# Kernel optimization log

Measured on AMD Instinct MI355X. Metric: run time of the kernel, lower is better.

The kernel has to match this reference:

```python
import jax, jax.numpy as jnp
import numpy as np

B, S, E, H = 4, 2048, 1024, 16
D = E // H  # head_dim = 64


def setup_inputs() -> dict:
    key = jax.random.key(0)
    ks = jax.random.split(key, 5)
    return {
        "x": jax.random.normal(ks[0], (B, S, E), dtype=jnp.float32),
        "w_qkv": jax.random.normal(ks[1], (3 * E, E), dtype=jnp.float32) * (E ** -0.5),
        "b_qkv": jax.random.normal(ks[2], (3 * E,), dtype=jnp.float32) * 0.02,
        "w_proj": jax.random.normal(ks[3], (E, E), dtype=jnp.float32) * (E ** -0.5),
        "b_proj": jax.random.normal(ks[4], (E,), dtype=jnp.float32) * 0.02,
    }


def reference(x, w_qkv, b_qkv, w_proj, b_proj):
    # fused QKV projection: [B,S,E] -> [B,S,3E] -> [B,S,3,H,D]
    qkv = (jnp.einsum("bse,fe->bsf", x, w_qkv) + b_qkv).reshape(B, S, 3, H, D)
    q, k, v = qkv[:, :, 0], qkv[:, :, 1], qkv[:, :, 2]  # each [B,S,H,D]
    scale = 1.0 / jnp.sqrt(jnp.asarray(D, dtype=q.dtype))
    scores = jnp.einsum("bqhd,bkhd->bhqk", q, k) * scale  # [B,H,S,S]
    attn = jax.nn.softmax(scores, axis=-1)
    out = jnp.einsum("bhqk,bkhd->bqhd", attn, v).reshape(B, S, E)
    return jnp.einsum("bse,fe->bsf", out, w_proj) + b_proj
```

## Files before the change

kernel.cpp:

```cpp
#include <hip/hip_runtime.h>
#include <cstdint>
#include <cstddef>

#define B_ 4
#define S_ 2048
#define E_ 1024
#define H_ 16
#define D_ 64
#define M_ (B_*S_)
#define NE_ ((size_t)B_*H_*S_*D_)

typedef unsigned int  u32;
typedef unsigned short u16;
typedef __attribute__((ext_vector_type(8))) short bf16x8;
typedef __attribute__((ext_vector_type(4))) float f32x4;
typedef __attribute__((ext_vector_type(2))) unsigned int u32x2;

__device__ __forceinline__ u16 f2bf(float x) {
    u32 u = __float_as_uint(x);
    u32 r = (u + 0x7FFFu + ((u >> 16) & 1u)) >> 16;
    return (u16)r;
}
__device__ __forceinline__ float bf2f(u16 h) { return __uint_as_float((u32)h << 16); }

__device__ __forceinline__ u32 cvtpk_bf16(float lo, float hi) {
    u32 r;
    asm("v_cvt_pk_bf16_f32 %0, %1, %2" : "=v"(r) : "v"(lo), "v"(hi));
    return r;
}

__device__ __forceinline__ void gload_lds16(const void* gsrc, void* lds) {
    __builtin_amdgcn_global_load_lds(
        (const __attribute__((address_space(1))) u32*)gsrc,
        (__attribute__((address_space(3))) u32*)lds, 16, 0, 0);
}


__global__ __launch_bounds__(256)
void convert_img(const float* __restrict__ src, u16* __restrict__ dh, u16* __restrict__ dl)
{
    const int tile = blockIdx.x;
    const int rt = tile >> 5, kt = tile & 31;
    const size_t tb = (size_t)tile * 2048;
    const int ci = threadIdx.x;
    const int l  = ci >> 3;
    const int ph = ci & 7;
    const int s  = ph ^ (l & 7);
    const int r  = (l << 1) | (s >> 2);
    const int k0 = (s & 3) << 3;
    const float* sp = src + ((size_t)(rt * 64 + r)) * 1024 + kt * 32 + k0;
    const float4 f0 = *(const float4*)sp;
    const float4 f1 = *(const float4*)(sp + 4);
    const float vals[8] = {f0.x, f0.y, f0.z, f0.w, f1.x, f1.y, f1.z, f1.w};
    __align__(16) short hs[8];
    __align__(16) short ls[8];
    #pragma unroll
    for (int j = 0; j < 8; ++j) {
        const u16 h = f2bf(vals[j]);
        hs[j] = (short)h;
        ls[j] = (short)f2bf(vals[j] - bf2f(h));
    }
    *(bf16x8*)(dh + tb + ci * 8) = *(const bf16x8*)hs;
    *(bf16x8*)(dl + tb + ci * 8) = *(const bf16x8*)ls;
}

template<int MODE>
__global__ __launch_bounds__(512, 1)
void gemm_mfma(const u16* __restrict__ AIh, const u16* __restrict__ AIl,
               const u16* __restrict__ BIh, const u16* __restrict__ BIl,
               const float* __restrict__ bias, float* __restrict__ Cout,
               u16* __restrict__ qh, u16* __restrict__ ql,
               u16* __restrict__ kh,
               u16* __restrict__ vh, u16* __restrict__ vl)
{
    __shared__ __align__(16) u16 sT[3][12][2048];

    constexpr int GY = (MODE == 0) ? 24 : 8;
    constexpr int NCH = (32 * GY) >> 3;

    const int tid = threadIdx.x, lane = tid & 63, w = tid >> 6;
    const int quad = lane >> 4, l15 = lane & 15;

    const int flat = blockIdx.x;
    const int swz  = (flat & 7) * NCH + (flat >> 3);
    const int bx   = swz / GY, by = swz % GY;

    const int m0  = bx * 256;
    const int n0  = by * 128;
    const int mt0 = bx * 4;
    const int nt0 = by * 2;
    const int rw  = w >> 1;
    const int cw  = w & 1;

    const u16* srcq[6];
    #pragma unroll
    for (int it = 0; it < 6; ++it) {
        const int g = w * 6 + it;
        const int t = g >> 2, qtr = g & 3;
        const u16* img = (t < 4) ? AIh : (t < 8) ? AIl : (t < 10) ? BIh : BIl;
        const int rtile = (t < 8) ? (mt0 + (t & 3)) : (nt0 + (t & 1));
        srcq[it] = img + (size_t)rtile * (32 * 2048) + qtr * 512 + lane * 8;
    }

    f32x4 acc[4][4];
    #pragma unroll
    for (int i = 0; i < 4; ++i)
        #pragma unroll
        for (int j = 0; j < 4; ++j)
            acc[i][j] = (f32x4){0.f, 0.f, 0.f, 0.f};

    #pragma unroll
    for (int it = 0; it < 6; ++it)
        gload_lds16(srcq[it], (char*)&sT[0][0][0] + (w * 6 + it) * 1024);
    #pragma unroll
    for (int it = 0; it < 6; ++it)
        gload_lds16(srcq[it] + 2048, (char*)&sT[1][0][0] + (w * 6 + it) * 1024);

    int cb = 0;
    for (int kt = 0; kt < 32; ++kt) {
        if (kt < 31) asm volatile("s_waitcnt vmcnt(6)" ::: "memory");
        else         asm volatile("s_waitcnt vmcnt(0)" ::: "memory");
        asm volatile("s_barrier" ::: "memory");

        if (kt + 2 < 32) {
            int nb = cb + 2; if (nb >= 3) nb -= 3;
            #pragma unroll
            for (int it = 0; it < 6; ++it)
                gload_lds16(srcq[it] + (size_t)(kt + 2) * 2048,
                            (char*)&sT[nb][0][0] + (w * 6 + it) * 1024);
        }

        bf16x8 aH[4], aL[4], bH[4], bL[4];
        #pragma unroll
        for (int i = 0; i < 4; ++i) {
            const int r = i * 16 + l15, l = r >> 1;
            const int off = l * 64 + (((((r & 1) << 2) + quad) ^ (l & 7)) << 3);
            aH[i] = *(const bf16x8*)&sT[cb][rw][off];
            aL[i] = *(const bf16x8*)&sT[cb][4 + rw][off];
        }
        #pragma unroll
        for (int j = 0; j < 4; ++j) {
            const int r = j * 16 + l15, l = r >> 1;
            const int off = l * 64 + (((((r & 1) << 2) + quad) ^ (l & 7)) << 3);
            bH[j] = *(const bf16x8*)&sT[cb][8 + cw][off];
            bL[j] = *(const bf16x8*)&sT[cb][10 + cw][off];
        }

        __builtin_amdgcn_s_setprio(1);
        #pragma unroll
        for (int i = 0; i < 4; ++i)
            #pragma unroll
            for (int j = 0; j < 4; ++j) {
                acc[i][j] = __builtin_amdgcn_mfma_f32_16x16x32_bf16(aL[i], bH[j], acc[i][j], 0, 0, 0);
                acc[i][j] = __builtin_amdgcn_mfma_f32_16x16x32_bf16(aH[i], bL[j], acc[i][j], 0, 0, 0);
                acc[i][j] = __builtin_amdgcn_mfma_f32_16x16x32_bf16(aH[i], bH[j], acc[i][j], 0, 0, 0);
            }
        __builtin_amdgcn_s_setprio(0);

        cb += 1; if (cb >= 3) cb = 0;
    }

    const int fbase = n0 + cw * 64;
    float bj[4];
    #pragma unroll
    for (int j = 0; j < 4; ++j) bj[j] = bias[fbase + j * 16 + l15];

    if (MODE == 0) {
        const int cR = fbase >> 10;
        const int hh = (fbase >> 6) & 15;
        #pragma unroll
        for (int i = 0; i < 4; ++i)
            #pragma unroll
            for (int j = 0; j < 4; ++j)
                #pragma unroll
                for (int reg = 0; reg < 4; ++reg) {
                    float val = acc[i][j][reg] + bj[j];
                    const int m = m0 + rw * 64 + i * 16 + quad * 4 + reg;
                    const int d = j * 16 + l15;
                    const int bb = m >> 11, s = m & 2047;
                    const int bh = bb * 16 + hh;
                    if (cR == 0) val *= 0.18033688011112042f;
                    const u16 h = f2bf(val);
                    if (cR == 0) {
                        const u16 lo = f2bf(val - bf2f(h));
                        const size_t idx = ((size_t)bh * 2048 + s) * 64 + d;
                        qh[idx] = h; ql[idx] = lo;
                    } else if (cR == 1) {
                        const size_t tile = (size_t)bh * 32 + (s >> 6);
                        const int r = s & 63;
                        const size_t off = (tile << 12) + r * 64 + (((d >> 3) ^ (r & 7)) << 3) + (d & 7);
                        kh[off] = h;
                    } else {
                        const u16 lo = f2bf(val - bf2f(h));
                        const size_t tile = (size_t)bh * 32 + (s >> 6);
                        const size_t off = (tile << 12) + d * 64 + ((((s & 63) >> 3) ^ (d & 7)) << 3) + (s & 7);
                        vh[off] = h; vl[off] = lo;
                    }
                }
    } else {
        #pragma unroll
        for (int i = 0; i < 4; ++i)
            #pragma unroll
            for (int j = 0; j < 4; ++j)
                #pragma unroll
                for (int reg = 0; reg < 4; ++reg) {
                    const int m = m0 + rw * 64 + i * 16 + quad * 4 + reg;
                    const int f = fbase + j * 16 + l15;
                    Cout[(size_t)m * 1024 + f] = acc[i][j][reg] + bj[j];
                }
    }
}

__global__ __launch_bounds__(256, 3)
void attn_mfma(const u16* __restrict__ qh, const u16* __restrict__ ql,
               const u16* __restrict__ kh,
               const u16* __restrict__ vh, const u16* __restrict__ vl,
               u16* __restrict__ oh, u16* __restrict__ ol)
{
    __shared__ __align__(16) u16 KV[3][4096];

    const int tid  = threadIdx.x;
    const int lane = tid & 63, w = tid >> 6;
    const int quad = lane >> 4, l15 = lane & 15;
    const int bh = blockIdx.y;
    const int q0 = blockIdx.x * 128 + w * 32;

    bf16x8 Qf[2][2][2];
    #pragma unroll
    for (int qs = 0; qs < 2; ++qs)
        #pragma unroll
        for (int kk = 0; kk < 2; ++kk) {
            const size_t idx = ((size_t)bh * S_ + q0 + qs * 16 + l15) * 64 + kk * 32 + quad * 8;
            Qf[qs][kk][0] = *(const bf16x8*)(qh + idx);
            Qf[qs][kk][1] = *(const bf16x8*)(ql + idx);
        }

    f32x4 O[2][4];
    float l_part[2] = {0.f, 0.f};
    #pragma unroll
    for (int qs = 0; qs < 2; ++qs)
        #pragma unroll
        for (int ds = 0; ds < 4; ++ds)
            O[qs][ds] = (f32x4){0.f, 0.f, 0.f, 0.f};

    const char* gk[3] = {(const char*)kh, (const char*)vh, (const char*)vl};

    for (int kt = 0; kt < S_ / 64; ++kt) {
        __syncthreads();
        const size_t tb = (((size_t)bh * 32 + kt) << 13);
        #pragma unroll
        for (int a = 0; a < 3; ++a)
            #pragma unroll
            for (int it = 0; it < 2; ++it) {
                const int off = w * 2048 + it * 1024;
                gload_lds16(gk[a] + tb + off + lane * 16, (char*)&KV[a][0] + off);
            }
        __syncthreads();

        f32x4 S[2][4];
        #pragma unroll
        for (int qs = 0; qs < 2; ++qs)
            #pragma unroll
            for (int ks = 0; ks < 4; ++ks)
                S[qs][ks] = (f32x4){-23.083120654223414f, -23.083120654223414f,
                                    -23.083120654223414f, -23.083120654223414f};

        __builtin_amdgcn_s_setprio(1);
        #pragma unroll
        for (int ks = 0; ks < 4; ++ks) {
            const int r = ks * 16 + l15;
            #pragma unroll
            for (int kk = 0; kk < 2; ++kk) {
                const int c = (kk * 4 + quad) ^ (r & 7);
                const bf16x8 Kh = *(const bf16x8*)&KV[0][r * 64 + c * 8];
                #pragma unroll
                for (int qs = 0; qs < 2; ++qs) {
                    S[qs][ks] = __builtin_amdgcn_mfma_f32_16x16x32_bf16(Kh, Qf[qs][kk][1], S[qs][ks], 0, 0, 0);
                    S[qs][ks] = __builtin_amdgcn_mfma_f32_16x16x32_bf16(Kh, Qf[qs][kk][0], S[qs][ks], 0, 0, 0);
                }
            }
        }
        __builtin_amdgcn_s_setprio(0);

        u32 PA[2][2][4];
        #pragma unroll
        for (int qs = 0; qs < 2; ++qs) {
            float lsum = 0.f;
            u32 PK[4][2];
            #pragma unroll
            for (int ks = 0; ks < 4; ++ks) {
                const float p0 = __builtin_exp2f(S[qs][ks][0]);
                const float p1 = __builtin_exp2f(S[qs][ks][1]);
                const float p2 = __builtin_exp2f(S[qs][ks][2]);
                const float p3 = __builtin_exp2f(S[qs][ks][3]);
                lsum += (p0 + p1) + (p2 + p3);
                PK[ks][0] = cvtpk_bf16(p0, p1);
                PK[ks][1] = cvtpk_bf16(p2, p3);
            }
            l_part[qs] += lsum;
            #pragma unroll
            for (int kk = 0; kk < 2; ++kk) {
                const u32x2 t0 = __builtin_amdgcn_permlane32_swap(PK[2 * kk][0], PK[2 * kk + 1][0], false, false);
                const u32x2 w02 = __builtin_amdgcn_permlane16_swap(t0.x, t0.y, false, false);
                const u32x2 t1 = __builtin_amdgcn_permlane32_swap(PK[2 * kk][1], PK[2 * kk + 1][1], false, false);
                const u32x2 w13 = __builtin_amdgcn_permlane16_swap(t1.x, t1.y, false, false);
                PA[qs][kk][0] = w02.x;
                PA[qs][kk][1] = w13.x;
                PA[qs][kk][2] = w02.y;
                PA[qs][kk][3] = w13.y;
            }
        }

        __builtin_amdgcn_s_setprio(1);
        #pragma unroll
        for (int kk = 0; kk < 2; ++kk) {
            union { u32 w4[4]; bf16x8 v; } pu0, pu1;
            #pragma unroll
            for (int c = 0; c < 4; ++c) { pu0.w4[c] = PA[0][kk][c]; pu1.w4[c] = PA[1][kk][c]; }
            const bf16x8 paf[2] = {pu0.v, pu1.v};
            #pragma unroll
            for (int ds = 0; ds < 4; ++ds) {
                const int r = ds * 16 + l15;
                const int c = (kk * 4 + quad) ^ (r & 7);
                const bf16x8 Vh = *(const bf16x8*)&KV[1][r * 64 + c * 8];
                const bf16x8 Vl = *(const bf16x8*)&KV[2][r * 64 + c * 8];
                #pragma unroll
                for (int qs = 0; qs < 2; ++qs) {
                    O[qs][ds] = __builtin_amdgcn_mfma_f32_16x16x32_bf16(Vl, paf[qs], O[qs][ds], 0, 0, 0);
                    O[qs][ds] = __builtin_amdgcn_mfma_f32_16x16x32_bf16(Vh, paf[qs], O[qs][ds], 0, 0, 0);
                }
            }
        }
        __builtin_amdgcn_s_setprio(0);
    }

    float linv[2];
    #pragma unroll
    for (int qs = 0; qs < 2; ++qs) {
        float rs = l_part[qs];
        rs += __shfl_xor(rs, 16);
        rs += __shfl_xor(rs, 32);
        linv[qs] = 1.f / rs;
    }

    const int bb = bh >> 4, hh = bh & 15;
    #pragma unroll
    for (int qs = 0; qs < 2; ++qs) {
        const float inv = linv[qs];
        const int s = q0 + qs * 16 + l15;
        const int m = bb * 2048 + s;
        const int mt = m >> 6, r = m & 63;
        const int l = r >> 1;
        const size_t tb0 = ((size_t)(mt * 32 + hh * 2)) * 2048;
        #pragma unroll
        for (int ds = 0; ds < 4; ++ds) {
            const int d0 = ds * 16 + quad * 4;
            const float v0 = O[qs][ds][0] * inv;
            const float v1 = O[qs][ds][1] * inv;
            const float v2 = O[qs][ds][2] * inv;
            const float v3 = O[qs][ds][3] * inv;
            const u32 h01 = cvtpk_bf16(v0, v1);
            const u32 h23 = cvtpk_bf16(v2, v3);
            const float r0 = v0 - bf2f((u16)h01);
            const float r1 = v1 - bf2f((u16)(h01 >> 16));
            const float r2 = v2 - bf2f((u16)h23);
            const float r3 = v3 - bf2f((u16)(h23 >> 16));
            const u32 l01 = cvtpk_bf16(r0, r1);
            const u32 l23 = cvtpk_bf16(r2, r3);
            const int c  = (d0 & 31) >> 3;
            const int ph = (((r & 1) << 2) + c) ^ (l & 7);
            const size_t off = tb0 + (size_t)(d0 >> 5) * 2048 + l * 64 + ph * 8 + (d0 & 7);
            *(u32x2*)(oh + off) = (u32x2){h01, h23};
            *(u32x2*)(ol + off) = (u32x2){l01, l23};
        }
    }
}

extern "C" void kernel_launch(void* const* d_in, const int* in_sizes, int n_in,
                              void* d_out, int out_size, void* d_ws, size_t ws_size,
                              hipStream_t stream) {
    const float* x      = (const float*)d_in[0];
    const float* w_qkv  = (const float*)d_in[1];
    const float* b_qkv  = (const float*)d_in[2];
    const float* w_proj = (const float*)d_in[3];
    const float* b_proj = (const float*)d_in[4];
    float* out = (float*)d_out;

    u16* qh  = (u16*)d_ws;
    u16* ql  = qh + NE_;
    u16* kh  = ql + NE_;
    u16* vh  = kh + NE_;
    u16* vl  = vh + NE_;
    u16* xh  = vl + NE_;
    u16* xl  = xh + NE_;
    u16* wqh = xl + NE_;
    u16* wql = wqh + (size_t)3 * 1024 * 1024;
    u16* oh  = xh;
    u16* ol  = xl;
    u16* wph = wqh;
    u16* wpl = wph + (size_t)1024 * 1024;

    convert_img<<<128 * 32, 256, 0, stream>>>(x, xh, xl);
    convert_img<<<48 * 32, 256, 0, stream>>>(w_qkv, wqh, wql);

    {
        dim3 grid(32 * 24);
        gemm_mfma<0><<<grid, 512, 0, stream>>>(xh, xl, wqh, wql,
                                               b_qkv, nullptr, qh, ql, kh, vh, vl);
    }
    {
        dim3 grid(S_ / 128, B_ * H_);
        attn_mfma<<<grid, 256, 0, stream>>>(qh, ql, kh, vh, vl, oh, ol);
    }
    convert_img<<<16 * 32, 256, 0, stream>>>(w_proj, wph, wpl);
    {
        dim3 grid(32 * 8);
        gemm_mfma<1><<<grid, 512, 0, stream>>>(oh, ol, wph, wpl,
                                               b_proj, out, nullptr, nullptr, nullptr,
                                               nullptr, nullptr);
    }
}
```

Before: 444.3 us.

## Split output projection into dedicated double-buffered GEMM kernel with two blocks per CU

The templated GEMM is split into a QKV kernel and a separate projection kernel. The projection kernel uses a two-stage LDS buffer instead of three, which frees enough shared memory for launch bounds of two 512-thread blocks per CU. It also drops the swizzled 1D grid in favour of a plain 2D grid and syncs every k-step. The aim is more occupancy on the small 256-block projection GEMM, at the cost of less prefetch depth and an extra barrier per iteration.

```diff
diff --git a/kernel.cpp b/kernel.cpp
--- a/kernel.cpp
+++ b/kernel.cpp
@@ -64,18 +64,17 @@
     *(bf16x8*)(dl + tb + ci * 8) = *(const bf16x8*)ls;
 }
 
-template<int MODE>
 __global__ __launch_bounds__(512, 1)
-void gemm_mfma(const u16* __restrict__ AIh, const u16* __restrict__ AIl,
-               const u16* __restrict__ BIh, const u16* __restrict__ BIl,
-               const float* __restrict__ bias, float* __restrict__ Cout,
-               u16* __restrict__ qh, u16* __restrict__ ql,
-               u16* __restrict__ kh,
-               u16* __restrict__ vh, u16* __restrict__ vl)
+void gemm_qkv(const u16* __restrict__ AIh, const u16* __restrict__ AIl,
+              const u16* __restrict__ BIh, const u16* __restrict__ BIl,
+              const float* __restrict__ bias,
+              u16* __restrict__ qh, u16* __restrict__ ql,
+              u16* __restrict__ kh,
+              u16* __restrict__ vh, u16* __restrict__ vl)
 {
     __shared__ __align__(16) u16 sT[3][12][2048];
 
-    constexpr int GY = (MODE == 0) ? 24 : 8;
+    constexpr int GY = 24;
     constexpr int NCH = (32 * GY) >> 3;
 
     const int tid = threadIdx.x, lane = tid & 63, w = tid >> 6;
@@ -165,50 +164,129 @@
     #pragma unroll
     for (int j = 0; j < 4; ++j) bj[j] = bias[fbase + j * 16 + l15];
 
-    if (MODE == 0) {
-        const int cR = fbase >> 10;
-        const int hh = (fbase >> 6) & 15;
+    const int cR = fbase >> 10;
+    const int hh = (fbase >> 6) & 15;
+    #pragma unroll
+    for (int i = 0; i < 4; ++i)
+        #pragma unroll
+        for (int j = 0; j < 4; ++j)
+            #pragma unroll
+            for (int reg = 0; reg < 4; ++reg) {
+                float val = acc[i][j][reg] + bj[j];
+                const int m = m0 + rw * 64 + i * 16 + quad * 4 + reg;
+                const int d = j * 16 + l15;
+                const int bb = m >> 11, s = m & 2047;
+                const int bh = bb * 16 + hh;
+                if (cR == 0) val *= 0.18033688011112042f;
+                const u16 h = f2bf(val);
+                if (cR == 0) {
+                    const u16 lo = f2bf(val - bf2f(h));
+                    const size_t idx = ((size_t)bh * 2048 + s) * 64 + d;
+                    qh[idx] = h; ql[idx] = lo;
+                } else if (cR == 1) {
+                    const size_t tile = (size_t)bh * 32 + (s >> 6);
+                    const int r = s & 63;
+                    const size_t off = (tile << 12) + r * 64 + (((d >> 3) ^ (r & 7)) << 3) + (d & 7);
+                    kh[off] = h;
+                } else {
+                    const u16 lo = f2bf(val - bf2f(h));
+                    const size_t tile = (size_t)bh * 32 + (s >> 6);
+                    const size_t off = (tile << 12) + d * 64 + ((((s & 63) >> 3) ^ (d & 7)) << 3) + (s & 7);
+                    vh[off] = h; vl[off] = lo;
+                }
+            }
+}
+
+__global__ __launch_bounds__(512, 2)
+void gemm_proj(const u16* __restrict__ AIh, const u16* __restrict__ AIl,
+               const u16* __restrict__ BIh, const u16* __restrict__ BIl,
+               const float* __restrict__ bias, float* __restrict__ Cout)
+{
+    __shared__ __align__(16) u16 sT[2][12][2048];
+
+    const int tid = threadIdx.x, lane = tid & 63, w = tid >> 6;
+    const int quad = lane >> 4, l15 = lane & 15;
+    const int bx = blockIdx.x, by = blockIdx.y;
+    const int m0  = bx * 256;
+    const int n0  = by * 128;
+    const int mt0 = bx * 4;
+    const int nt0 = by * 2;
+    const int rw  = w >> 1;
+    const int cw  = w & 1;
+
+    const u16* srcq[6];
+    #pragma unroll
+    for (int it = 0; it < 6; ++it) {
+        const int g = w * 6 + it;
+        const int t = g >> 2, qtr = g & 3;
+        const u16* img = (t < 4) ? AIh : (t < 8) ? AIl : (t < 10) ? BIh : BIl;
+        const int rtile = (t < 8) ? (mt0 + (t & 3)) : (nt0 + (t & 1));
+        srcq[it] = img + (size_t)rtile * (32 * 2048) + qtr * 512 + lane * 8;
+    }
+
+    f32x4 acc[4][4];
+    #pragma unroll
+    for (int i = 0; i < 4; ++i)
+        #pragma unroll
+        for (int j = 0; j < 4; ++j)
+            acc[i][j] = (f32x4){0.f, 0.f, 0.f, 0.f};
+
+    #pragma unroll
+    for (int it = 0; it < 6; ++it)
+        gload_lds16(srcq[it], (char*)&sT[0][0][0] + (w * 6 + it) * 1024);
+    __syncthreads();
+
+    #pragma unroll 2
+    for (int kt = 0; kt < 32; ++kt) {
+        const int cur = kt & 1;
+        bf16x8 aH[4], aL[4], bH[4], bL[4];
+        #pragma unroll
+        for (int i = 0; i < 4; ++i) {
+            const int r = i * 16 + l15, l = r >> 1;
+            const int off = l * 64 + (((((r & 1) << 2) + quad) ^ (l & 7)) << 3);
+            aH[i] = *(const bf16x8*)&sT[cur][rw][off];
+            aL[i] = *(const bf16x8*)&sT[cur][4 + rw][off];
+        }
+        #pragma unroll
+        for (int j = 0; j < 4; ++j) {
+            const int r = j * 16 + l15, l = r >> 1;
+            const int off = l * 64 + (((((r & 1) << 2) + quad) ^ (l & 7)) << 3);
+            bH[j] = *(const bf16x8*)&sT[cur][8 + cw][off];
+            bL[j] = *(const bf16x8*)&sT[cur][10 + cw][off];
+        }
+        if (kt < 31) {
+            #pragma unroll
+            for (int it = 0; it < 6; ++it)
+                gload_lds16(srcq[it] + (size_t)(kt + 1) * 2048,
+                            (char*)&sT[cur ^ 1][0][0] + (w * 6 + it) * 1024);
+        }
+        __builtin_amdgcn_s_setprio(1);
         #pragma unroll
         for (int i = 0; i < 4; ++i)
             #pragma unroll
-            for (int j = 0; j < 4; ++j)
-                #pragma unroll
-                for (int reg = 0; reg < 4; ++reg) {
-                    float val = acc[i][j][reg] + bj[j];
-                    const int m = m0 + rw * 64 + i * 16 + quad * 4 + reg;
-                    const int d = j * 16 + l15;
-                    const int bb = m >> 11, s = m & 2047;
-                    const int bh = bb * 16 + hh;
-                    if (cR == 0) val *= 0.18033688011112042f;
-                    const u16 h = f2bf(val);
-                    if (cR == 0) {
-                        const u16 lo = f2bf(val - bf2f(h));
-                        const size_t idx = ((size_t)bh * 2048 + s) * 64 + d;
-                        qh[idx] = h; ql[idx] = lo;
-                    } else if (cR == 1) {
-                        const size_t tile = (size_t)bh * 32 + (s >> 6);
-                        const int r = s & 63;
-                        const size_t off = (tile << 12) + r * 64 + (((d >> 3) ^ (r & 7)) << 3) + (d & 7);
-                        kh[off] = h;
-                    } else {
-                        const u16 lo = f2bf(val - bf2f(h));
-                        const size_t tile = (size_t)bh * 32 + (s >> 6);
-                        const size_t off = (tile << 12) + d * 64 + ((((s & 63) >> 3) ^ (d & 7)) << 3) + (s & 7);
-                        vh[off] = h; vl[off] = lo;
-                    }
-                }
-    } else {
-        #pragma unroll
-        for (int i = 0; i < 4; ++i)
-            #pragma unroll
-            for (int j = 0; j < 4; ++j)
-                #pragma unroll
-                for (int reg = 0; reg < 4; ++reg) {
-                    const int m = m0 + rw * 64 + i * 16 + quad * 4 + reg;
-                    const int f = fbase + j * 16 + l15;
-                    Cout[(size_t)m * 1024 + f] = acc[i][j][reg] + bj[j];
-                }
-    }
+            for (int j = 0; j < 4; ++j) {
+                acc[i][j] = __builtin_amdgcn_mfma_f32_16x16x32_bf16(aL[i], bH[j], acc[i][j], 0, 0, 0);
+                acc[i][j] = __builtin_amdgcn_mfma_f32_16x16x32_bf16(aH[i], bL[j], acc[i][j], 0, 0, 0);
+                acc[i][j] = __builtin_amdgcn_mfma_f32_16x16x32_bf16(aH[i], bH[j], acc[i][j], 0, 0, 0);
+            }
+        __builtin_amdgcn_s_setprio(0);
+        __syncthreads();
+    }
+
+    const int fbase = n0 + cw * 64;
+    float bj[4];
+    #pragma unroll
+    for (int j = 0; j < 4; ++j) bj[j] = bias[fbase + j * 16 + l15];
+    #pragma unroll
+    for (int i = 0; i < 4; ++i)
+        #pragma unroll
+        for (int j = 0; j < 4; ++j)
+            #pragma unroll
+            for (int reg = 0; reg < 4; ++reg) {
+                const int m = m0 + rw * 64 + i * 16 + quad * 4 + reg;
+                const int f = fbase + j * 16 + l15;
+                Cout[(size_t)m * 1024 + f] = acc[i][j][reg] + bj[j];
+            }
 }
 
 __global__ __launch_bounds__(256, 3)
@@ -405,8 +483,8 @@
 
     {
         dim3 grid(32 * 24);
-        gemm_mfma<0><<<grid, 512, 0, stream>>>(xh, xl, wqh, wql,
-                                               b_qkv, nullptr, qh, ql, kh, vh, vl);
+        gemm_qkv<<<grid, 512, 0, stream>>>(xh, xl, wqh, wql,
+                                           b_qkv, qh, ql, kh, vh, vl);
     }
     {
         dim3 grid(S_ / 128, B_ * H_);
@@ -414,9 +492,7 @@
     }
     convert_img<<<16 * 32, 256, 0, stream>>>(w_proj, wph, wpl);
     {
-        dim3 grid(32 * 8);
-        gemm_mfma<1><<<grid, 512, 0, stream>>>(oh, ol, wph, wpl,
-                                               b_proj, out, nullptr, nullptr, nullptr,
-                                               nullptr, nullptr);
-    }
-}
+        dim3 grid(M_ / 256, E_ / 128);
+        gemm_proj<<<grid, 512, 0, stream>>>(oh, ol, wph, wpl, b_proj, out);
+    }
+}
```

After: 443.3 us. Within noise of the previous version (-0.2%).
